# Optimization experiments

Hardware: AMD Instinct MI355X
Metric: run time of the kernel (lower is better)

## Reference

```python
import jax, jax.numpy as jnp
import numpy as np

N = 50000
D_IN = 128
HID = 128
HEADS = 4
PER_HEAD = HID // HEADS
NEG_SLOPE = 0.2


def gatv2_conv(x, src, dst, W_l, W_r, att, bias, H, C, n):
    """PyG GATv2Conv: x [n,F], src/dst [E] (self-loops already appended).
    out[i] = sum_{j->i} softmax_i(att . leaky_relu(Wl x_j + Wr x_i)) * (Wl x_j)
    """
    x_l = (x @ W_l).reshape(n, H, C)  # source-side transform
    x_r = (x @ W_r).reshape(n, H, C)  # destination-side transform
    e = jax.nn.leaky_relu(x_l[src] + x_r[dst], NEG_SLOPE)      # [E,H,C]
    alpha = jnp.einsum('ehc,hc->eh', e, att)                    # [E,H]
    # segment softmax over incoming edges of each destination node
    seg_max = jax.ops.segment_max(alpha, dst, num_segments=n)   # [n,H]
    alpha = jnp.exp(alpha - seg_max[dst])
    denom = jax.ops.segment_sum(alpha, dst, num_segments=n)     # [n,H]
    alpha = alpha / denom[dst]
    msg = x_l[src] * alpha[..., None]                           # [E,H,C]
    out = jax.ops.segment_sum(msg, dst, num_segments=n)         # [n,H,C]
    return out.reshape(n, H * C) + bias


def setup_inputs() -> dict:
    key = jax.random.key(0)
    ks = jax.random.split(key, 10)
    E = 800000
    x = jax.random.normal(ks[0], (N, D_IN), dtype=jnp.float32)
    edge_index = jax.random.randint(ks[1], (2, E), 0, N, dtype=jnp.int64)

    def glorot(k, shape):
        lim = float(np.sqrt(6.0 / (shape[0] + shape[1])))
        return jax.random.uniform(k, shape, jnp.float32, -lim, lim)

    # layer 1: GATv2Conv(D_IN, PER_HEAD, heads=HEADS, concat=True)
    W_l1 = glorot(ks[2], (D_IN, HEADS * PER_HEAD))
    W_r1 = glorot(ks[3], (D_IN, HEADS * PER_HEAD))
    att1 = glorot(ks[4], (HEADS, PER_HEAD))
    b1 = jnp.zeros((HEADS * PER_HEAD,), jnp.float32)
    # layer 2: GATv2Conv(HID, HID, heads=1, concat=True)
    W_l2 = glorot(ks[5], (HID, HID))
    W_r2 = glorot(ks[6], (HID, HID))
    att2 = glorot(ks[7], (1, HID))
    b2 = jnp.zeros((HID,), jnp.float32)
    return {"x": x, "edge_index": edge_index,
            "W_l1": W_l1, "W_r1": W_r1, "att1": att1, "b1": b1,
            "W_l2": W_l2, "W_r2": W_r2, "att2": att2, "b2": b2}


def reference(x, edge_index, W_l1, W_r1, att1, b1, W_l2, W_r2, att2, b2):
    # add self-loops (PyG GATv2Conv default add_self_loops=True)
    loops = jnp.arange(N, dtype=edge_index.dtype)
    src = jnp.concatenate([edge_index[0], loops])
    dst = jnp.concatenate([edge_index[1], loops])
    h = gatv2_conv(x, src, dst, W_l1, W_r1, att1, b1, HEADS, PER_HEAD, N)
    h = jax.nn.relu(h)
    out = gatv2_conv(h, src, dst, W_l2, W_r2, att2, b2, 1, HID, N)
    return out
```

## Files before the change

### kernel.cpp

```cpp
#include <hip/hip_runtime.h>
#include <hip/hip_fp16.h>
#include <math.h>


#define NEG_SLOPE 0.2f
#define CHUNKS 128
#define DCAP 8192

typedef _Float16 half8 __attribute__((ext_vector_type(8)));
typedef _Float16 half2v __attribute__((ext_vector_type(2)));
typedef float floatx4 __attribute__((ext_vector_type(4)));

#if defined(__has_builtin)
#if __has_builtin(__builtin_amdgcn_fdot2)
#define HAVE_FDOT2 1
#endif
#endif

template <int CTRL>
__device__ __forceinline__ float dppmov(float x) {
    int xi = __builtin_bit_cast(int, x);
    int r  = __builtin_amdgcn_update_dpp(0, xi, CTRL, 0xF, 0xF, true);
    return __builtin_bit_cast(float, r);
}
#define DPP_XOR1  0xB1
#define DPP_XOR2  0x4E
#define DPP_HMIRR 0x141
#define DPP_MIRR  0x140


__device__ __forceinline__ void sortA_body(int c, const int* __restrict__ dstA,
                                           int* __restrict__ hist_mat,
                                           int E, int Et, int csz) {
    __shared__ int hist[256];
    int tid = threadIdx.x;
    hist[tid] = 0;
    __syncthreads();
    int start = c * csz, stop = min(Et, start + csz);
    for (int e = start + tid; e < stop; e += 256) {
        int d = (e < E) ? dstA[e] : (e - E);
        atomicAdd(&hist[d >> 8], 1);
    }
    __syncthreads();
    hist_mat[tid * CHUNKS + c] = hist[tid];
}

__device__ __forceinline__ void convert_body(int t,
        const float* __restrict__ Wl1, const float* __restrict__ Wr1,
        const float* __restrict__ Wl2, const float* __restrict__ Wr2,
        const float* __restrict__ att1, const float* __restrict__ att2,
        _Float16* __restrict__ Wt1, _Float16* __restrict__ Wt2,
        _Float16* __restrict__ attH) {
    if (t < 65536) {
        int layer = t >> 15;
        int id = t & 32767;
        int c = id >> 7, k = id & 127;
        const float* Wl = layer ? Wl2 : Wl1;
        const float* Wr = layer ? Wr2 : Wr1;
        _Float16* Wt = layer ? Wt2 : Wt1;
        float v = (c < 128) ? Wl[(size_t)k * 128 + c] : Wr[(size_t)k * 128 + (c - 128)];
        Wt[(size_t)c * 128 + k] = (_Float16)v;
    } else {
        int id = t - 65536;
        if (id < 256) {
            float v = (id < 128) ? att1[id] : att2[id - 128];
            attH[id] = (_Float16)v;
        }
    }
}

__device__ __forceinline__ void scan256_body(const int* __restrict__ hist_mat,
                                             int* __restrict__ offs_flat) {
    __shared__ int wsum[4];
    int t = threadIdx.x;
    int lane = t & 63, w = t >> 6;
    const int4* hp = (const int4*)hist_mat + t * 32;
    int local = 0;
    #pragma unroll 8
    for (int j = 0; j < 32; ++j) {
        int4 v = hp[j];
        local += v.x + v.y + v.z + v.w;
    }
    int x = local;
    #pragma unroll
    for (int off = 1; off < 64; off <<= 1) {
        int y = __shfl_up(x, off, 64);
        if (lane >= off) x += y;
    }
    if (lane == 63) wsum[w] = x;
    __syncthreads();
    int woff = 0;
    for (int i = 0; i < w; ++i) woff += wsum[i];
    int run = woff + x - local;
    int4* op = (int4*)offs_flat + t * 32;
    #pragma unroll 8
    for (int j = 0; j < 32; ++j) {
        int4 v = hp[j];
        int4 o;
        o.x = run;
        o.y = run + v.x;
        o.z = o.y + v.y;
        o.w = o.z + v.z;
        run = o.w + v.w;
        op[j] = o;
    }
}

__device__ __forceinline__ void sortC_body(int c, const int* __restrict__ srcA,
        const int* __restrict__ dstA, const int* __restrict__ offs_flat,
        int* __restrict__ packed, int E, int Et, int csz) {
    __shared__ int pos[256];
    int tid = threadIdx.x;
    pos[tid] = offs_flat[tid * CHUNKS + c];
    __syncthreads();
    int start = c * csz, stop = min(Et, start + csz);
    for (int e = start + tid; e < stop; e += 256) {
        int s, d;
        if (e < E) { s = srcA[e]; d = dstA[e]; } else { s = e - E; d = s; }
        int p = atomicAdd(&pos[d >> 8], 1);
        packed[p] = ((d & 255) << 16) | s;
    }
}

#define BPAD 136

template <bool AF32>
__device__ __forceinline__ void gemm_body(int bid, const void* __restrict__ Av,
        const _Float16* __restrict__ Bt, _Float16* __restrict__ outL,
        _Float16* __restrict__ outR, int n) {
    __shared__ _Float16 sB[256 * BPAD];
    int tid = threadIdx.x;
    {
        int c0 = (tid & 15) * 8;
        int r0 = tid >> 4;
        #pragma unroll
        for (int i = 0; i < 16; ++i) {
            int r = r0 + i * 16;
            *(half8*)(sB + r * BPAD + c0) = *(const half8*)(Bt + (size_t)r * 128 + c0);
        }
    }
    int wave = tid >> 6;
    int lane = tid & 63;
    int ln = lane & 15;
    int q  = lane >> 4;
    int row0 = bid * 64 + wave * 16;

    int arow = row0 + ln;
    if (arow >= n) arow = n - 1;
    half8 a0, a1, a2, a3;
    if (AF32) {
        const float* ap = (const float*)Av + (size_t)arow * 128 + q * 8;
        #pragma unroll
        for (int g = 0; g < 4; ++g) {
            float4 f0 = *(const float4*)(ap + g * 32);
            float4 f1 = *(const float4*)(ap + g * 32 + 4);
            half8 h;
            h[0] = (_Float16)f0.x; h[1] = (_Float16)f0.y;
            h[2] = (_Float16)f0.z; h[3] = (_Float16)f0.w;
            h[4] = (_Float16)f1.x; h[5] = (_Float16)f1.y;
            h[6] = (_Float16)f1.z; h[7] = (_Float16)f1.w;
            if (g == 0) a0 = h; else if (g == 1) a1 = h;
            else if (g == 2) a2 = h; else a3 = h;
        }
    } else {
        const _Float16* ap = (const _Float16*)Av + (size_t)arow * 128 + q * 8;
        a0 = *(const half8*)(ap);
        a1 = *(const half8*)(ap + 32);
        a2 = *(const half8*)(ap + 64);
        a3 = *(const half8*)(ap + 96);
    }

    __syncthreads();

    floatx4 acc[16];
    #pragma unroll
    for (int ct = 0; ct < 16; ++ct) {
        const _Float16* bp = sB + (ct * 16 + ln) * BPAD + q * 8;
        half8 b0 = *(const half8*)(bp);
        half8 b1 = *(const half8*)(bp + 32);
        half8 b2 = *(const half8*)(bp + 64);
        half8 b3 = *(const half8*)(bp + 96);
        floatx4 c = {0.f, 0.f, 0.f, 0.f};
        c = __builtin_amdgcn_mfma_f32_16x16x32_f16(a0, b0, c, 0, 0, 0);
        c = __builtin_amdgcn_mfma_f32_16x16x32_f16(a1, b1, c, 0, 0, 0);
        c = __builtin_amdgcn_mfma_f32_16x16x32_f16(a2, b2, c, 0, 0, 0);
        c = __builtin_amdgcn_mfma_f32_16x16x32_f16(a3, b3, c, 0, 0, 0);
        acc[ct] = c;
    }

    #pragma unroll
    for (int ct = 0; ct < 16; ++ct) {
        int col = ct * 16 + ln;
        #pragma unroll
        for (int r = 0; r < 4; ++r) {
            int grow = row0 + q * 4 + r;
            if (grow < n) {
                _Float16 v = (_Float16)acc[ct][r];
                if (ct < 8) outL[(size_t)grow * 128 + col] = v;
                else        outR[(size_t)grow * 128 + (col - 128)] = v;
            }
        }
    }
}


__global__ __launch_bounds__(256)
void fused_pre(const int* __restrict__ dstA, int* __restrict__ hist_mat,
               int E, int Et, int csz,
               const float* __restrict__ Wl1, const float* __restrict__ Wr1,
               const float* __restrict__ Wl2, const float* __restrict__ Wr2,
               const float* __restrict__ att1, const float* __restrict__ att2,
               _Float16* __restrict__ Wt1, _Float16* __restrict__ Wt2,
               _Float16* __restrict__ attH) {
    if (blockIdx.x < CHUNKS) {
        sortA_body(blockIdx.x, dstA, hist_mat, E, Et, csz);
    } else {
        int t = (blockIdx.x - CHUNKS) * 256 + threadIdx.x;
        convert_body(t, Wl1, Wr1, Wl2, Wr2, att1, att2, Wt1, Wt2, attH);
    }
}

__global__ __launch_bounds__(256)
void fused_scan_gemm(const int* __restrict__ hist_mat, int* __restrict__ offs_flat,
                     const float* __restrict__ X, const _Float16* __restrict__ Wt1,
                     _Float16* __restrict__ outL, _Float16* __restrict__ outR, int n) {
    if (blockIdx.x == 0) {
        scan256_body(hist_mat, offs_flat);
    } else {
        gemm_body<true>(blockIdx.x - 1, X, Wt1, outL, outR, n);
    }
}

__global__ __launch_bounds__(256)
void fused_mid(const int* __restrict__ srcA, const int* __restrict__ dstA,
               const int* __restrict__ offs_flat, int* __restrict__ packed,
               int E, int Et, int csz, int gemm_base,
               const float* __restrict__ X, const _Float16* __restrict__ Wt1,
               _Float16* __restrict__ outL, _Float16* __restrict__ outR, int n) {
    if (blockIdx.x < CHUNKS) {
        sortC_body(blockIdx.x, srcA, dstA, offs_flat, packed, E, Et, csz);
    } else {
        gemm_body<true>(blockIdx.x - CHUNKS + gemm_base, X, Wt1, outL, outR, n);
    }
}

__global__ __launch_bounds__(256)
void gemm_l2(const _Float16* __restrict__ A, const _Float16* __restrict__ Bt,
             _Float16* __restrict__ outL, _Float16* __restrict__ outR, int n) {
    gemm_body<false>(blockIdx.x, A, Bt, outL, outR, n);
}

__global__ __launch_bounds__(256)
void sortD_fine(const int* __restrict__ offs_flat, const int* __restrict__ packed,
                int* __restrict__ rowptr, int* __restrict__ srcs,
                int n, int Et, int nbuck) {
    __shared__ int stage[DCAP];
    __shared__ int sorted[DCAP];
    __shared__ int hist[256], curv[256], wsumD[4];
    int tid = threadIdx.x, b = blockIdx.x;
    int base = offs_flat[b * CHUNKS];
    int end  = (b == nbuck - 1) ? Et : offs_flat[(b + 1) * CHUNKS];
    int m = min(end - base, DCAP);

    hist[tid] = 0;
    for (int i = tid; i < m; i += 256) stage[i] = packed[base + i];
    __syncthreads();
    for (int i = tid; i < m; i += 256) atomicAdd(&hist[stage[i] >> 16], 1);
    __syncthreads();
    {
        int v = hist[tid];
        int lane = tid & 63, w = tid >> 6;
        int x = v;
        #pragma unroll
        for (int off = 1; off < 64; off <<= 1) {
            int y = __shfl_up(x, off, 64);
            if (lane >= off) x += y;
        }
        if (lane == 63) wsumD[w] = x;
        __syncthreads();
        int woff = 0;
        for (int i = 0; i < w; ++i) woff += wsumD[i];
        int excl = woff + x - v;
        curv[tid] = excl;
        int node0 = b << 8;
        if (node0 + tid < n) rowptr[node0 + tid] = base + excl;
        if (b == 0 && tid == 0) rowptr[n] = Et;
    }
    __syncthreads();
    for (int i = tid; i < m; i += 256) {
        int p = stage[i];
        int pos = atomicAdd(&curv[p >> 16], 1);
        sorted[pos] = p & 0xFFFF;
    }
    __syncthreads();
    for (int i = tid; i < m; i += 256) srcs[base + i] = sorted[i];
}


template <bool LAYER1>
__global__ __launch_bounds__(256)
void edge_aggregate(const _Float16* __restrict__ xl, const _Float16* __restrict__ xr,
                    const _Float16* __restrict__ attH, const float* __restrict__ bias,
                    const int* __restrict__ rowptr, const int* __restrict__ srcs,
                    void* __restrict__ outv, int n) {
    int node = blockIdx.x * (blockDim.x >> 6) + (threadIdx.x >> 6);
    int lane = threadIdx.x & 63;
    if (node >= n) return;
    int ln = lane & 15;
    int q  = lane >> 4;
    int c0 = ln * 8;

    half8 xrh = *(const half8*)(xr + (size_t)node * 128 + c0);
    half8 ahh = *(const half8*)(attH + c0);

    float acc[8] = {0.f, 0.f, 0.f, 0.f, 0.f, 0.f, 0.f, 0.f};
    float l = 0.f;

    auto proc = [&](half8 vh, bool valid) {
        half8 e  = vh + xrh;
        half8 es = e * (_Float16)NEG_SLOPE;
        half8 lr = __builtin_elementwise_max(e, es);
        float p = 0.f;
        #pragma unroll
        for (int k = 0; k < 4; ++k) {
            half2v ee = { lr[2 * k], lr[2 * k + 1] };
            half2v aa = { ahh[2 * k], ahh[2 * k + 1] };
#ifdef HAVE_FDOT2
            p = __builtin_amdgcn_fdot2(ee, aa, p, false);
#else
            p = fmaf((float)ee[0], (float)aa[0], p);
            p = fmaf((float)ee[1], (float)aa[1], p);
#endif
        }
        p += dppmov<DPP_XOR1>(p);
        p += dppmov<DPP_XOR2>(p);
        if (!LAYER1) { p += dppmov<DPP_HMIRR>(p); p += dppmov<DPP_MIRR>(p); }
        float pe = __expf(p);
        if (!valid) pe = 0.f;
        l += pe;
        #pragma unroll
        for (int k = 0; k < 8; ++k) acc[k] = fmaf(pe, (float)vh[k], acc[k]);
    };

    int jb = rowptr[node], je = rowptr[node + 1];
    for (int base = jb; base < je; base += 64) {
        int idx = base + lane;
        int myS = (idx < je) ? srcs[idx] : 0;
        int cnt = min(64, je - base);
        int t = 0;
        for (; t + 16 <= cnt; t += 16) {
            int s0 = __shfl(myS, t + q, 64);
            int s1 = __shfl(myS, t + 4 + q, 64);
            int s2 = __shfl(myS, t + 8 + q, 64);
            int s3 = __shfl(myS, t + 12 + q, 64);
            half8 v0 = *(const half8*)(xl + (size_t)s0 * 128 + c0);
            half8 v1 = *(const half8*)(xl + (size_t)s1 * 128 + c0);
            half8 v2 = *(const half8*)(xl + (size_t)s2 * 128 + c0);
            half8 v3 = *(const half8*)(xl + (size_t)s3 * 128 + c0);
            proc(v0, true); proc(v1, true); proc(v2, true); proc(v3, true);
        }
        for (; t < cnt; t += 4) {
            int sa = __shfl(myS, t + q, 64);
            half8 va = *(const half8*)(xl + (size_t)sa * 128 + c0);
            proc(va, (t + q) < cnt);
        }
    }

    #pragma unroll
    for (int k = 0; k < 8; ++k) {
        acc[k] += __shfl_xor(acc[k], 16, 64);
        acc[k] += __shfl_xor(acc[k], 32, 64);
    }
    l += __shfl_xor(l, 16, 64);
    l += __shfl_xor(l, 32, 64);

    float inv = 1.0f / l;
    float bv[8];
    *(float4*)&bv[0] = *(const float4*)(bias + c0);
    *(float4*)&bv[4] = *(const float4*)(bias + c0 + 4);
    float o[8];
    #pragma unroll
    for (int k = 0; k < 8; ++k) {
        o[k] = acc[k] * inv + bv[k];
        if (LAYER1) o[k] = fmaxf(o[k], 0.f);
    }
    if (lane < 16) {
        if (LAYER1) {
            __half2 hh2[4];
            #pragma unroll
            for (int k = 0; k < 4; ++k) hh2[k] = __floats2half2_rn(o[2 * k], o[2 * k + 1]);
            *(float4*)((_Float16*)outv + (size_t)node * 128 + c0) = *(float4*)&hh2[0];
        } else {
            float* out = (float*)outv;
            *(float4*)(out + (size_t)node * 128 + c0)     = *(float4*)&o[0];
            *(float4*)(out + (size_t)node * 128 + c0 + 4) = *(float4*)&o[4];
        }
    }
}


extern "C" void kernel_launch(void* const* d_in, const int* in_sizes, int n_in,
                              void* d_out, int out_size, void* d_ws, size_t ws_size,
                              hipStream_t stream) {
    const float* x    = (const float*)d_in[0];
    const int*   ei   = (const int*)d_in[1];
    const float* Wl1  = (const float*)d_in[2];
    const float* Wr1  = (const float*)d_in[3];
    const float* att1 = (const float*)d_in[4];
    const float* b1   = (const float*)d_in[5];
    const float* Wl2  = (const float*)d_in[6];
    const float* Wr2  = (const float*)d_in[7];
    const float* att2 = (const float*)d_in[8];
    const float* b2   = (const float*)d_in[9];

    int n  = in_sizes[0] / 128;
    int E  = in_sizes[1] / 2;
    int Et = E + n;

    _Float16* xlh  = (_Float16*)d_ws;
    _Float16* xrh2 = xlh + (size_t)n * 128;
    _Float16* hh   = xrh2 + (size_t)n * 128;
    _Float16* Wt1  = hh  + (size_t)n * 128;
    _Float16* Wt2  = Wt1 + 256 * 128;
    _Float16* attH = Wt2 + 256 * 128;
    int* rowptr   = (int*)(attH + 256);
    int* srcs     = rowptr + ((n + 4) & ~3);
    int* packed   = srcs + Et;
    int* hist_mat = packed + Et;
    int* offs_flat= hist_mat + CHUNKS * 256;

    const int* srcA = ei;
    const int* dstA = ei + E;

    int csz   = (Et + CHUNKS - 1) / CHUNKS;
    int nbuck = (n + 255) >> 8;
    int gemm_grid = (n + 63) / 64;
    int edge_grid = (n + 3) / 4;
    int GA = gemm_grid >> 1;
    int GB = gemm_grid - GA;

    fused_pre<<<CHUNKS + 257, 256, 0, stream>>>(
        dstA, hist_mat, E, Et, csz,
        Wl1, Wr1, Wl2, Wr2, att1, att2, Wt1, Wt2, attH);
    fused_scan_gemm<<<1 + GA, 256, 0, stream>>>(
        hist_mat, offs_flat, x, Wt1, xlh, xrh2, n);
    fused_mid<<<CHUNKS + GB, 256, 0, stream>>>(
        srcA, dstA, offs_flat, packed, E, Et, csz, GA,
        x, Wt1, xlh, xrh2, n);
    sortD_fine<<<nbuck, 256, 0, stream>>>(offs_flat, packed, rowptr, srcs, n, Et, nbuck);
    edge_aggregate<true><<<edge_grid, 256, 0, stream>>>(
        xlh, xrh2, attH, b1, rowptr, srcs, hh, n);
    gemm_l2<<<gemm_grid, 256, 0, stream>>>(hh, Wt2, xlh, xrh2, n);
    edge_aggregate<false><<<edge_grid, 256, 0, stream>>>(
        xlh, xrh2, attH + 128, b2, rowptr, srcs, d_out, n);
}
```

Baseline: 217.4 us.

## Replace two-level bucket sort with global-atomic counting sort for CSR build

Swaps the two-pass bucket sort (per-chunk 256-bucket histograms, then a per-bucket fine sort in LDS) for a direct counting sort. Per-node degrees are counted with global atomics, a single block scans them into rowptr and a cursor array, and a scatter pass writes sources through global atomics on the cursor. This drops the sortD_fine kernel and the packed intermediate buffer but adds a memset and many contended global atomics. The order of sources within each row becomes nondeterministic, and the scan now runs on a single block over all nodes.

```diff
diff --git a/kernel.cpp b/kernel.cpp
--- a/kernel.cpp
+++ b/kernel.cpp
@@ -4,8 +4,8 @@
 
 
 #define NEG_SLOPE 0.2f
-#define CHUNKS 128
-#define DCAP 8192
+#define COUNTB 128
+#define SCATB  128
 
 typedef _Float16 half8 __attribute__((ext_vector_type(8)));
 typedef _Float16 half2v __attribute__((ext_vector_type(2)));
@@ -29,20 +29,13 @@
 #define DPP_MIRR  0x140
 
 
-__device__ __forceinline__ void sortA_body(int c, const int* __restrict__ dstA,
-                                           int* __restrict__ hist_mat,
-                                           int E, int Et, int csz) {
-    __shared__ int hist[256];
-    int tid = threadIdx.x;
-    hist[tid] = 0;
-    __syncthreads();
-    int start = c * csz, stop = min(Et, start + csz);
-    for (int e = start + tid; e < stop; e += 256) {
+__device__ __forceinline__ void count_body(int b, const int* __restrict__ dstA,
+                                           int* __restrict__ counts, int E, int Et) {
+    const int STR = COUNTB * 256;
+    for (int e = b * 256 + threadIdx.x; e < Et; e += STR) {
         int d = (e < E) ? dstA[e] : (e - E);
-        atomicAdd(&hist[d >> 8], 1);
-    }
-    __syncthreads();
-    hist_mat[tid * CHUNKS + c] = hist[tid];
+        atomicAdd(&counts[d], 1);
+    }
 }
 
 __device__ __forceinline__ void convert_body(int t,
@@ -69,16 +62,16 @@
     }
 }
 
-__device__ __forceinline__ void scan256_body(const int* __restrict__ hist_mat,
-                                             int* __restrict__ offs_flat) {
+__device__ __forceinline__ void scan_body(const int* __restrict__ counts,
+        int* __restrict__ rowptr, int* __restrict__ cursor, int n, int Et) {
     __shared__ int wsum[4];
     int t = threadIdx.x;
     int lane = t & 63, w = t >> 6;
-    const int4* hp = (const int4*)hist_mat + t * 32;
+    int c4 = (n + 1023) >> 10;
+    const int4* cp = (const int4*)counts + (size_t)t * c4;
     int local = 0;
-    #pragma unroll 8
-    for (int j = 0; j < 32; ++j) {
-        int4 v = hp[j];
+    for (int j = 0; j < c4; ++j) {
+        int4 v = cp[j];
         local += v.x + v.y + v.z + v.w;
     }
     int x = local;
@@ -92,33 +85,48 @@
     int woff = 0;
     for (int i = 0; i < w; ++i) woff += wsum[i];
     int run = woff + x - local;
-    int4* op = (int4*)offs_flat + t * 32;
-    #pragma unroll 8
-    for (int j = 0; j < 32; ++j) {
-        int4 v = hp[j];
+    int4* rp = (int4*)rowptr + (size_t)t * c4;
+    int4* qp = (int4*)cursor + (size_t)t * c4;
+    for (int j = 0; j < c4; ++j) {
+        int4 v = cp[j];
         int4 o;
         o.x = run;
         o.y = run + v.x;
         o.z = o.y + v.y;
         o.w = o.z + v.z;
         run = o.w + v.w;
-        op[j] = o;
-    }
-}
-
-__device__ __forceinline__ void sortC_body(int c, const int* __restrict__ srcA,
-        const int* __restrict__ dstA, const int* __restrict__ offs_flat,
-        int* __restrict__ packed, int E, int Et, int csz) {
-    __shared__ int pos[256];
-    int tid = threadIdx.x;
-    pos[tid] = offs_flat[tid * CHUNKS + c];
-    __syncthreads();
-    int start = c * csz, stop = min(Et, start + csz);
-    for (int e = start + tid; e < stop; e += 256) {
+        rp[j] = o;
+        qp[j] = o;
+    }
+    if (t == 255) rowptr[n] = Et;
+}
+
+__device__ __forceinline__ void scatter_body(int b, const int* __restrict__ srcA,
+        const int* __restrict__ dstA, int* __restrict__ cursor,
+        int* __restrict__ srcs, int E, int Et) {
+    const int STR = SCATB * 256;
+    int e = b * 256 + threadIdx.x;
+    for (; e + 3 * STR < Et; e += 4 * STR) {
+        int ea = e, eb = e + STR, ec = e + 2 * STR, ed = e + 3 * STR;
+        int s0, d0, s1, d1, s2, d2, s3, d3;
+        if (ea < E) { s0 = srcA[ea]; d0 = dstA[ea]; } else { s0 = ea - E; d0 = s0; }
+        if (eb < E) { s1 = srcA[eb]; d1 = dstA[eb]; } else { s1 = eb - E; d1 = s1; }
+        if (ec < E) { s2 = srcA[ec]; d2 = dstA[ec]; } else { s2 = ec - E; d2 = s2; }
+        if (ed < E) { s3 = srcA[ed]; d3 = dstA[ed]; } else { s3 = ed - E; d3 = s3; }
+        int p0 = atomicAdd(&cursor[d0], 1);
+        int p1 = atomicAdd(&cursor[d1], 1);
+        int p2 = atomicAdd(&cursor[d2], 1);
+        int p3 = atomicAdd(&cursor[d3], 1);
+        srcs[p0] = s0;
+        srcs[p1] = s1;
+        srcs[p2] = s2;
+        srcs[p3] = s3;
+    }
+    for (; e < Et; e += STR) {
         int s, d;
         if (e < E) { s = srcA[e]; d = dstA[e]; } else { s = e - E; d = s; }
-        int p = atomicAdd(&pos[d >> 8], 1);
-        packed[p] = ((d & 255) << 16) | s;
+        int p = atomicAdd(&cursor[d], 1);
+        srcs[p] = s;
     }
 }
 
@@ -205,42 +213,45 @@
 
 
 __global__ __launch_bounds__(256)
-void fused_pre(const int* __restrict__ dstA, int* __restrict__ hist_mat,
-               int E, int Et, int csz,
+void fused_pre(const int* __restrict__ dstA, int* __restrict__ counts,
+               int E, int Et,
                const float* __restrict__ Wl1, const float* __restrict__ Wr1,
                const float* __restrict__ Wl2, const float* __restrict__ Wr2,
                const float* __restrict__ att1, const float* __restrict__ att2,
                _Float16* __restrict__ Wt1, _Float16* __restrict__ Wt2,
                _Float16* __restrict__ attH) {
-    if (blockIdx.x < CHUNKS) {
-        sortA_body(blockIdx.x, dstA, hist_mat, E, Et, csz);
+    if (blockIdx.x < COUNTB) {
+        count_body(blockIdx.x, dstA, counts, E, Et);
     } else {
-        int t = (blockIdx.x - CHUNKS) * 256 + threadIdx.x;
+        int t = (blockIdx.x - COUNTB) * 256 + threadIdx.x;
         convert_body(t, Wl1, Wr1, Wl2, Wr2, att1, att2, Wt1, Wt2, attH);
     }
 }
 
 __global__ __launch_bounds__(256)
-void fused_scan_gemm(const int* __restrict__ hist_mat, int* __restrict__ offs_flat,
+void fused_scan_gemm(const int* __restrict__ counts, int* __restrict__ rowptr,
+                     int* __restrict__ cursor,
                      const float* __restrict__ X, const _Float16* __restrict__ Wt1,
-                     _Float16* __restrict__ outL, _Float16* __restrict__ outR, int n) {
+                     _Float16* __restrict__ outL, _Float16* __restrict__ outR,
+                     int n, int Et) {
     if (blockIdx.x == 0) {
-        scan256_body(hist_mat, offs_flat);
+        scan_body(counts, rowptr, cursor, n, Et);
     } else {
         gemm_body<true>(blockIdx.x - 1, X, Wt1, outL, outR, n);
     }
 }
 
 __global__ __launch_bounds__(256)
-void fused_mid(const int* __restrict__ srcA, const int* __restrict__ dstA,
-               const int* __restrict__ offs_flat, int* __restrict__ packed,
-               int E, int Et, int csz, int gemm_base,
-               const float* __restrict__ X, const _Float16* __restrict__ Wt1,
-               _Float16* __restrict__ outL, _Float16* __restrict__ outR, int n) {
-    if (blockIdx.x < CHUNKS) {
-        sortC_body(blockIdx.x, srcA, dstA, offs_flat, packed, E, Et, csz);
+void fused_scatter_gemm(const int* __restrict__ srcA, const int* __restrict__ dstA,
+                        int* __restrict__ cursor, int* __restrict__ srcs,
+                        int E, int Et, int gemm_base,
+                        const float* __restrict__ X, const _Float16* __restrict__ Wt1,
+                        _Float16* __restrict__ outL, _Float16* __restrict__ outR,
+                        int n) {
+    if (blockIdx.x < SCATB) {
+        scatter_body(blockIdx.x, srcA, dstA, cursor, srcs, E, Et);
     } else {
-        gemm_body<true>(blockIdx.x - CHUNKS + gemm_base, X, Wt1, outL, outR, n);
+        gemm_body<true>(blockIdx.x - SCATB + gemm_base, X, Wt1, outL, outR, n);
     }
 }
 
@@ -248,52 +259,6 @@
 void gemm_l2(const _Float16* __restrict__ A, const _Float16* __restrict__ Bt,
              _Float16* __restrict__ outL, _Float16* __restrict__ outR, int n) {
     gemm_body<false>(blockIdx.x, A, Bt, outL, outR, n);
-}
-
-__global__ __launch_bounds__(256)
-void sortD_fine(const int* __restrict__ offs_flat, const int* __restrict__ packed,
-                int* __restrict__ rowptr, int* __restrict__ srcs,
-                int n, int Et, int nbuck) {
-    __shared__ int stage[DCAP];
-    __shared__ int sorted[DCAP];
-    __shared__ int hist[256], curv[256], wsumD[4];
-    int tid = threadIdx.x, b = blockIdx.x;
-    int base = offs_flat[b * CHUNKS];
-    int end  = (b == nbuck - 1) ? Et : offs_flat[(b + 1) * CHUNKS];
-    int m = min(end - base, DCAP);
-
-    hist[tid] = 0;
-    for (int i = tid; i < m; i += 256) stage[i] = packed[base + i];
-    __syncthreads();
-    for (int i = tid; i < m; i += 256) atomicAdd(&hist[stage[i] >> 16], 1);
-    __syncthreads();
-    {
-        int v = hist[tid];
-        int lane = tid & 63, w = tid >> 6;
-        int x = v;
-        #pragma unroll
-        for (int off = 1; off < 64; off <<= 1) {
-            int y = __shfl_up(x, off, 64);
-            if (lane >= off) x += y;
-        }
-        if (lane == 63) wsumD[w] = x;
-        __syncthreads();
-        int woff = 0;
-        for (int i = 0; i < w; ++i) woff += wsumD[i];
-        int excl = woff + x - v;
-        curv[tid] = excl;
-        int node0 = b << 8;
-        if (node0 + tid < n) rowptr[node0 + tid] = base + excl;
-        if (b == 0 && tid == 0) rowptr[n] = Et;
-    }
-    __syncthreads();
-    for (int i = tid; i < m; i += 256) {
-        int p = stage[i];
-        int pos = atomicAdd(&curv[p >> 16], 1);
-        sorted[pos] = p & 0xFFFF;
-    }
-    __syncthreads();
-    for (int i = tid; i < m; i += 256) srcs[base + i] = sorted[i];
 }
 
 
@@ -416,6 +381,7 @@
     int n  = in_sizes[0] / 128;
     int E  = in_sizes[1] / 2;
     int Et = E + n;
+    int npad = ((n + 1023) >> 10) << 10;
 
     _Float16* xlh  = (_Float16*)d_ws;
     _Float16* xrh2 = xlh + (size_t)n * 128;
@@ -423,31 +389,28 @@
     _Float16* Wt1  = hh  + (size_t)n * 128;
     _Float16* Wt2  = Wt1 + 256 * 128;
     _Float16* attH = Wt2 + 256 * 128;
-    int* rowptr   = (int*)(attH + 256);
-    int* srcs     = rowptr + ((n + 4) & ~3);
-    int* packed   = srcs + Et;
-    int* hist_mat = packed + Et;
-    int* offs_flat= hist_mat + CHUNKS * 256;
+    int* rowptr = (int*)(attH + 256);
+    int* cursor = rowptr + npad + 16;
+    int* counts = cursor + npad;
+    int* srcs   = counts + npad;
 
     const int* srcA = ei;
     const int* dstA = ei + E;
 
-    int csz   = (Et + CHUNKS - 1) / CHUNKS;
-    int nbuck = (n + 255) >> 8;
     int gemm_grid = (n + 63) / 64;
     int edge_grid = (n + 3) / 4;
     int GA = gemm_grid >> 1;
     int GB = gemm_grid - GA;
 
-    fused_pre<<<CHUNKS + 257, 256, 0, stream>>>(
-        dstA, hist_mat, E, Et, csz,
+    hipMemsetAsync(counts, 0, (size_t)npad * sizeof(int), stream);
+    fused_pre<<<COUNTB + 257, 256, 0, stream>>>(
+        dstA, counts, E, Et,
         Wl1, Wr1, Wl2, Wr2, att1, att2, Wt1, Wt2, attH);
     fused_scan_gemm<<<1 + GA, 256, 0, stream>>>(
-        hist_mat, offs_flat, x, Wt1, xlh, xrh2, n);
-    fused_mid<<<CHUNKS + GB, 256, 0, stream>>>(
-        srcA, dstA, offs_flat, packed, E, Et, csz, GA,
+        counts, rowptr, cursor, x, Wt1, xlh, xrh2, n, Et);
+    fused_scatter_gemm<<<SCATB + GB, 256, 0, stream>>>(
+        srcA, dstA, cursor, srcs, E, Et, GA,
         x, Wt1, xlh, xrh2, n);
-    sortD_fine<<<nbuck, 256, 0, stream>>>(offs_flat, packed, rowptr, srcs, n, Et, nbuck);
     edge_aggregate<true><<<edge_grid, 256, 0, stream>>>(
         xlh, xrh2, attH, b1, rowptr, srcs, hh, n);
     gemm_l2<<<gemm_grid, 256, 0, stream>>>(hh, Wt2, xlh, xrh2, n);
```

After: 287.2 us. 32.1% more time.

## Fuse fine bucket sort with layer-1 edge aggregation using 32-node buckets

Applied to the files above, without the earlier changes.

The coarse counting sort now uses 32-node buckets instead of 256-node ones, and 64 chunks instead of 128. The fine sort kernel is merged with the layer-1 attention aggregation, so each block sorts its bucket's sources into shared memory as 16-bit values and aggregates those nodes straight from shared memory. This removes one kernel launch and the global round trip of the sorted source list for layer 1. In exchange, the single-block scan now covers a much larger histogram, and each block's aggregation is limited to 32 nodes, with a shared-memory cap of 1024 edges per bucket.

```diff
diff --git a/kernel.cpp b/kernel.cpp
--- a/kernel.cpp
+++ b/kernel.cpp
@@ -4,8 +4,10 @@
 
 
 #define NEG_SLOPE 0.2f
-#define CHUNKS 128
-#define DCAP 8192
+#define CHUNKS 64
+#define NB 32
+#define NBUCK_PAD 2048
+#define DCAP 1024
 
 typedef _Float16 half8 __attribute__((ext_vector_type(8)));
 typedef _Float16 half2v __attribute__((ext_vector_type(2)));
@@ -32,17 +34,18 @@
 __device__ __forceinline__ void sortA_body(int c, const int* __restrict__ dstA,
                                            int* __restrict__ hist_mat,
                                            int E, int Et, int csz) {
-    __shared__ int hist[256];
+    __shared__ int hist[NBUCK_PAD];
     int tid = threadIdx.x;
-    hist[tid] = 0;
+    for (int k = tid; k < NBUCK_PAD; k += 256) hist[k] = 0;
     __syncthreads();
     int start = c * csz, stop = min(Et, start + csz);
     for (int e = start + tid; e < stop; e += 256) {
         int d = (e < E) ? dstA[e] : (e - E);
-        atomicAdd(&hist[d >> 8], 1);
-    }
-    __syncthreads();
-    hist_mat[tid * CHUNKS + c] = hist[tid];
+        atomicAdd(&hist[d >> 5], 1);
+    }
+    __syncthreads();
+    for (int k = tid; k < NBUCK_PAD; k += 256)
+        hist_mat[k * CHUNKS + c] = hist[k];
 }
 
 __device__ __forceinline__ void convert_body(int t,
@@ -69,15 +72,15 @@
     }
 }
 
-__device__ __forceinline__ void scan256_body(const int* __restrict__ hist_mat,
-                                             int* __restrict__ offs_flat) {
+__device__ __forceinline__ void scan_body(const int* __restrict__ hist_mat,
+                                          int* __restrict__ offs_flat) {
     __shared__ int wsum[4];
     int t = threadIdx.x;
     int lane = t & 63, w = t >> 6;
-    const int4* hp = (const int4*)hist_mat + t * 32;
+    const int4* hp = (const int4*)hist_mat + (size_t)t * 128;
     int local = 0;
     #pragma unroll 8
-    for (int j = 0; j < 32; ++j) {
+    for (int j = 0; j < 128; ++j) {
         int4 v = hp[j];
         local += v.x + v.y + v.z + v.w;
     }
@@ -92,9 +95,9 @@
     int woff = 0;
     for (int i = 0; i < w; ++i) woff += wsum[i];
     int run = woff + x - local;
-    int4* op = (int4*)offs_flat + t * 32;
+    int4* op = (int4*)offs_flat + (size_t)t * 128;
     #pragma unroll 8
-    for (int j = 0; j < 32; ++j) {
+    for (int j = 0; j < 128; ++j) {
         int4 v = hp[j];
         int4 o;
         o.x = run;
@@ -109,16 +112,17 @@
 __device__ __forceinline__ void sortC_body(int c, const int* __restrict__ srcA,
         const int* __restrict__ dstA, const int* __restrict__ offs_flat,
         int* __restrict__ packed, int E, int Et, int csz) {
-    __shared__ int pos[256];
+    __shared__ int pos[NBUCK_PAD];
     int tid = threadIdx.x;
-    pos[tid] = offs_flat[tid * CHUNKS + c];
+    for (int k = tid; k < NBUCK_PAD; k += 256)
+        pos[k] = offs_flat[k * CHUNKS + c];
     __syncthreads();
     int start = c * csz, stop = min(Et, start + csz);
     for (int e = start + tid; e < stop; e += 256) {
         int s, d;
         if (e < E) { s = srcA[e]; d = dstA[e]; } else { s = e - E; d = s; }
-        int p = atomicAdd(&pos[d >> 8], 1);
-        packed[p] = ((d & 255) << 16) | s;
+        int p = atomicAdd(&pos[d >> 5], 1);
+        packed[p] = ((d & 31) << 16) | s;
     }
 }
 
@@ -225,7 +229,7 @@
                      const float* __restrict__ X, const _Float16* __restrict__ Wt1,
                      _Float16* __restrict__ outL, _Float16* __restrict__ outR, int n) {
     if (blockIdx.x == 0) {
-        scan256_body(hist_mat, offs_flat);
+        scan_body(hist_mat, offs_flat);
     } else {
         gemm_body<true>(blockIdx.x - 1, X, Wt1, outL, outR, n);
     }
@@ -250,50 +254,138 @@
     gemm_body<false>(blockIdx.x, A, Bt, outL, outR, n);
 }
 
+
 __global__ __launch_bounds__(256)
-void sortD_fine(const int* __restrict__ offs_flat, const int* __restrict__ packed,
-                int* __restrict__ rowptr, int* __restrict__ srcs,
-                int n, int Et, int nbuck) {
+void sort_agg(const int* __restrict__ offs_flat, const int* __restrict__ packed,
+              int* __restrict__ rowptr, int* __restrict__ srcs,
+              const _Float16* __restrict__ xl, const _Float16* __restrict__ xr,
+              const _Float16* __restrict__ attH, const float* __restrict__ bias,
+              _Float16* __restrict__ out, int n, int Et) {
     __shared__ int stage[DCAP];
-    __shared__ int sorted[DCAP];
-    __shared__ int hist[256], curv[256], wsumD[4];
+    __shared__ unsigned short s16[DCAP];
+    __shared__ int hist[NB];
+    __shared__ int curv[NB];
+    __shared__ int rp_l[NB + 1];
+
     int tid = threadIdx.x, b = blockIdx.x;
     int base = offs_flat[b * CHUNKS];
-    int end  = (b == nbuck - 1) ? Et : offs_flat[(b + 1) * CHUNKS];
+    int end  = offs_flat[(b + 1) * CHUNKS];
     int m = min(end - base, DCAP);
-
-    hist[tid] = 0;
+    int node0 = b * NB;
+
+    if (tid < NB) hist[tid] = 0;
     for (int i = tid; i < m; i += 256) stage[i] = packed[base + i];
     __syncthreads();
     for (int i = tid; i < m; i += 256) atomicAdd(&hist[stage[i] >> 16], 1);
     __syncthreads();
-    {
-        int v = hist[tid];
-        int lane = tid & 63, w = tid >> 6;
+    if (tid < 64) {
+        int lane = tid;
+        int v = (lane < NB) ? hist[lane] : 0;
         int x = v;
         #pragma unroll
         for (int off = 1; off < 64; off <<= 1) {
             int y = __shfl_up(x, off, 64);
             if (lane >= off) x += y;
         }
-        if (lane == 63) wsumD[w] = x;
-        __syncthreads();
-        int woff = 0;
-        for (int i = 0; i < w; ++i) woff += wsumD[i];
-        int excl = woff + x - v;
-        curv[tid] = excl;
-        int node0 = b << 8;
-        if (node0 + tid < n) rowptr[node0 + tid] = base + excl;
-        if (b == 0 && tid == 0) rowptr[n] = Et;
+        if (lane < NB) { rp_l[lane] = x - v; curv[lane] = x - v; }
+        if (lane == NB - 1) rp_l[NB] = x;
     }
     __syncthreads();
     for (int i = tid; i < m; i += 256) {
         int p = stage[i];
         int pos = atomicAdd(&curv[p >> 16], 1);
-        sorted[pos] = p & 0xFFFF;
-    }
-    __syncthreads();
-    for (int i = tid; i < m; i += 256) srcs[base + i] = sorted[i];
+        s16[pos] = (unsigned short)(p & 0xFFFF);
+    }
+    __syncthreads();
+
+    if (tid < NB && node0 + tid < n) rowptr[node0 + tid] = base + rp_l[tid];
+    if (b == 0 && tid == 0) rowptr[n] = Et;
+    for (int i = tid; i < m; i += 256) srcs[base + i] = (int)s16[i];
+
+    int w = tid >> 6, lane = tid & 63;
+    int ln = lane & 15, q = lane >> 4, c0 = ln * 8;
+    half8 ahh = *(const half8*)(attH + c0);
+    float bv[8];
+    *(float4*)&bv[0] = *(const float4*)(bias + c0);
+    *(float4*)&bv[4] = *(const float4*)(bias + c0 + 4);
+
+    for (int i = 0; i < NB / 4; ++i) {
+        int j = w * (NB / 4) + i;
+        int node = node0 + j;
+        if (node >= n) break;
+        half8 xrh = *(const half8*)(xr + (size_t)node * 128 + c0);
+        float acc[8] = {0.f, 0.f, 0.f, 0.f, 0.f, 0.f, 0.f, 0.f};
+        float l = 0.f;
+
+        auto proc = [&](half8 vh, bool valid) {
+            half8 e  = vh + xrh;
+            half8 es = e * (_Float16)NEG_SLOPE;
+            half8 lr = __builtin_elementwise_max(e, es);
+            float p = 0.f;
+            #pragma unroll
+            for (int k = 0; k < 4; ++k) {
+                half2v ee = { lr[2 * k], lr[2 * k + 1] };
+                half2v aa = { ahh[2 * k], ahh[2 * k + 1] };
+#ifdef HAVE_FDOT2
+                p = __builtin_amdgcn_fdot2(ee, aa, p, false);
+#else
+                p = fmaf((float)ee[0], (float)aa[0], p);
+                p = fmaf((float)ee[1], (float)aa[1], p);
+#endif
+            }
+            p += dppmov<DPP_XOR1>(p);
+            p += dppmov<DPP_XOR2>(p);
+            float pe = __expf(p);
+            if (!valid) pe = 0.f;
+            l += pe;
+            #pragma unroll
+            for (int k = 0; k < 8; ++k) acc[k] = fmaf(pe, (float)vh[k], acc[k]);
+        };
+
+        int jb = rp_l[j], je = rp_l[j + 1];
+        for (int be = jb; be < je; be += 64) {
+            int idx = be + lane;
+            int myS = (idx < je) ? (int)s16[idx] : 0;
+            int cnt = min(64, je - be);
+            int t = 0;
+            for (; t + 16 <= cnt; t += 16) {
+                int s0 = __shfl(myS, t + q, 64);
+                int s1 = __shfl(myS, t + 4 + q, 64);
+                int s2 = __shfl(myS, t + 8 + q, 64);
+                int s3 = __shfl(myS, t + 12 + q, 64);
+                half8 v0 = *(const half8*)(xl + (size_t)s0 * 128 + c0);
+                half8 v1 = *(const half8*)(xl + (size_t)s1 * 128 + c0);
+                half8 v2 = *(const half8*)(xl + (size_t)s2 * 128 + c0);
+                half8 v3 = *(const half8*)(xl + (size_t)s3 * 128 + c0);
+                proc(v0, true); proc(v1, true); proc(v2, true); proc(v3, true);
+            }
+            for (; t < cnt; t += 4) {
+                int sa = __shfl(myS, t + q, 64);
+                half8 va = *(const half8*)(xl + (size_t)sa * 128 + c0);
+                proc(va, (t + q) < cnt);
+            }
+        }
+
+        #pragma unroll
+        for (int k = 0; k < 8; ++k) {
+            acc[k] += __shfl_xor(acc[k], 16, 64);
+            acc[k] += __shfl_xor(acc[k], 32, 64);
+        }
+        l += __shfl_xor(l, 16, 64);
+        l += __shfl_xor(l, 32, 64);
+
+        float inv = 1.0f / l;
+        float o[8];
+        #pragma unroll
+        for (int k = 0; k < 8; ++k)
+            o[k] = fmaxf(acc[k] * inv + bv[k], 0.f);
+        if (lane < 16) {
+            __half2 hh2[4];
+            #pragma unroll
+            for (int k = 0; k < 4; ++k) hh2[k] = __floats2half2_rn(o[2 * k], o[2 * k + 1]);
+            *(float4*)(out + (size_t)node * 128 + c0) = *(float4*)&hh2[0];
+        }
+    }
 }
 
 
@@ -424,16 +516,16 @@
     _Float16* Wt2  = Wt1 + 256 * 128;
     _Float16* attH = Wt2 + 256 * 128;
     int* rowptr   = (int*)(attH + 256);
-    int* srcs     = rowptr + ((n + 4) & ~3);
-    int* packed   = srcs + Et;
-    int* hist_mat = packed + Et;
-    int* offs_flat= hist_mat + CHUNKS * 256;
+    int* packed   = rowptr + ((n + 16) & ~3);
+    int* srcs     = packed + Et;
+    int* hist_mat = srcs + Et;
+    int* offs_flat= hist_mat + NBUCK_PAD * CHUNKS;
 
     const int* srcA = ei;
     const int* dstA = ei + E;
 
     int csz   = (Et + CHUNKS - 1) / CHUNKS;
-    int nbuck = (n + 255) >> 8;
+    int nbuck = (n + NB - 1) / NB;
     int gemm_grid = (n + 63) / 64;
     int edge_grid = (n + 3) / 4;
     int GA = gemm_grid >> 1;
@@ -447,9 +539,8 @@
     fused_mid<<<CHUNKS + GB, 256, 0, stream>>>(
         srcA, dstA, offs_flat, packed, E, Et, csz, GA,
         x, Wt1, xlh, xrh2, n);
-    sortD_fine<<<nbuck, 256, 0, stream>>>(offs_flat, packed, rowptr, srcs, n, Et, nbuck);
-    edge_aggregate<true><<<edge_grid, 256, 0, stream>>>(
-        xlh, xrh2, attH, b1, rowptr, srcs, hh, n);
+    sort_agg<<<nbuck, 256, 0, stream>>>(
+        offs_flat, packed, rowptr, srcs, xlh, xrh2, attH, b1, hh, n, Et);
     gemm_l2<<<gemm_grid, 256, 0, stream>>>(hh, Wt2, xlh, xrh2, n);
     edge_aggregate<false><<<edge_grid, 256, 0, stream>>>(
         xlh, xrh2, attH + 128, b2, rowptr, srcs, d_out, n);
```

Result: slower. 282.0 us (+29.7%).

## Fuse fine sort with a third slice of the layer-1 GEMM

Applied to the files above, without the earlier changes.

Splits the layer-1 GEMM into three slices instead of two and runs the last slice inside the fine-bucket sort kernel, so the sort's low-occupancy blocks overlap with GEMM blocks. The sort stage now keeps sorted sources as 16-bit values in dynamic shared memory that it shares with the GEMM's B tile, which fits both in about 68KB. The GEMM now receives its LDS buffer as a parameter. The risk is that the larger dynamic LDS allocation on every block limits occupancy, and that the GEMM slices may be unevenly balanced against the sort work.

```diff
diff --git a/kernel.cpp b/kernel.cpp
--- a/kernel.cpp
+++ b/kernel.cpp
@@ -122,13 +122,60 @@
     }
 }
 
+__device__ __forceinline__ void sortD_body(int b, const int* __restrict__ offs_flat,
+        const int* __restrict__ packed, int* __restrict__ rowptr,
+        int* __restrict__ srcs, int n, int Et, int nbuck, char* smem) {
+    int* stage = (int*)smem;
+    unsigned short* s16 = (unsigned short*)(smem + DCAP * 4);
+    int* hist  = (int*)(smem + DCAP * 6);
+    int* curv  = hist + 256;
+    int* wsumD = curv + 256;
+    int tid = threadIdx.x;
+    int base = offs_flat[b * CHUNKS];
+    int end  = (b == nbuck - 1) ? Et : offs_flat[(b + 1) * CHUNKS];
+    int m = min(end - base, DCAP);
+
+    hist[tid] = 0;
+    for (int i = tid; i < m; i += 256) stage[i] = packed[base + i];
+    __syncthreads();
+    for (int i = tid; i < m; i += 256) atomicAdd(&hist[stage[i] >> 16], 1);
+    __syncthreads();
+    {
+        int v = hist[tid];
+        int lane = tid & 63, w = tid >> 6;
+        int x = v;
+        #pragma unroll
+        for (int off = 1; off < 64; off <<= 1) {
+            int y = __shfl_up(x, off, 64);
+            if (lane >= off) x += y;
+        }
+        if (lane == 63) wsumD[w] = x;
+        __syncthreads();
+        int woff = 0;
+        for (int i = 0; i < w; ++i) woff += wsumD[i];
+        int excl = woff + x - v;
+        curv[tid] = excl;
+        int node0 = b << 8;
+        if (node0 + tid < n) rowptr[node0 + tid] = base + excl;
+        if (b == 0 && tid == 0) rowptr[n] = Et;
+    }
+    __syncthreads();
+    for (int i = tid; i < m; i += 256) {
+        int p = stage[i];
+        int pos = atomicAdd(&curv[p >> 16], 1);
+        s16[pos] = (unsigned short)(p & 0xFFFF);
+    }
+    __syncthreads();
+    for (int i = tid; i < m; i += 256) srcs[base + i] = (int)s16[i];
+}
+
 #define BPAD 136
+#define GEMM_LDS_BYTES (256 * BPAD * 2)
 
 template <bool AF32>
 __device__ __forceinline__ void gemm_body(int bid, const void* __restrict__ Av,
         const _Float16* __restrict__ Bt, _Float16* __restrict__ outL,
-        _Float16* __restrict__ outR, int n) {
-    __shared__ _Float16 sB[256 * BPAD];
+        _Float16* __restrict__ outR, int n, _Float16* sB) {
     int tid = threadIdx.x;
     {
         int c0 = (tid & 15) * 8;
@@ -224,10 +271,11 @@
 void fused_scan_gemm(const int* __restrict__ hist_mat, int* __restrict__ offs_flat,
                      const float* __restrict__ X, const _Float16* __restrict__ Wt1,
                      _Float16* __restrict__ outL, _Float16* __restrict__ outR, int n) {
+    __shared__ _Float16 sB[256 * BPAD];
     if (blockIdx.x == 0) {
         scan256_body(hist_mat, offs_flat);
     } else {
-        gemm_body<true>(blockIdx.x - 1, X, Wt1, outL, outR, n);
+        gemm_body<true>(blockIdx.x - 1, X, Wt1, outL, outR, n, sB);
     }
 }
 
@@ -237,63 +285,34 @@
                int E, int Et, int csz, int gemm_base,
                const float* __restrict__ X, const _Float16* __restrict__ Wt1,
                _Float16* __restrict__ outL, _Float16* __restrict__ outR, int n) {
+    __shared__ _Float16 sB[256 * BPAD];
     if (blockIdx.x < CHUNKS) {
         sortC_body(blockIdx.x, srcA, dstA, offs_flat, packed, E, Et, csz);
     } else {
-        gemm_body<true>(blockIdx.x - CHUNKS + gemm_base, X, Wt1, outL, outR, n);
+        gemm_body<true>(blockIdx.x - CHUNKS + gemm_base, X, Wt1, outL, outR, n, sB);
+    }
+}
+
+__global__ __launch_bounds__(256)
+void fused_sortD_gemm(const int* __restrict__ offs_flat, const int* __restrict__ packed,
+                      int* __restrict__ rowptr, int* __restrict__ srcs,
+                      int n, int Et, int nbuck, int gemm_base,
+                      const float* __restrict__ X, const _Float16* __restrict__ Wt1,
+                      _Float16* __restrict__ outL, _Float16* __restrict__ outR) {
+    extern __shared__ char smem[];
+    if (blockIdx.x < nbuck) {
+        sortD_body(blockIdx.x, offs_flat, packed, rowptr, srcs, n, Et, nbuck, smem);
+    } else {
+        gemm_body<true>(blockIdx.x - nbuck + gemm_base, X, Wt1, outL, outR, n,
+                        (_Float16*)smem);
     }
 }
 
 __global__ __launch_bounds__(256)
 void gemm_l2(const _Float16* __restrict__ A, const _Float16* __restrict__ Bt,
              _Float16* __restrict__ outL, _Float16* __restrict__ outR, int n) {
-    gemm_body<false>(blockIdx.x, A, Bt, outL, outR, n);
-}
-
-__global__ __launch_bounds__(256)
-void sortD_fine(const int* __restrict__ offs_flat, const int* __restrict__ packed,
-                int* __restrict__ rowptr, int* __restrict__ srcs,
-                int n, int Et, int nbuck) {
-    __shared__ int stage[DCAP];
-    __shared__ int sorted[DCAP];
-    __shared__ int hist[256], curv[256], wsumD[4];
-    int tid = threadIdx.x, b = blockIdx.x;
-    int base = offs_flat[b * CHUNKS];
-    int end  = (b == nbuck - 1) ? Et : offs_flat[(b + 1) * CHUNKS];
-    int m = min(end - base, DCAP);
-
-    hist[tid] = 0;
-    for (int i = tid; i < m; i += 256) stage[i] = packed[base + i];
-    __syncthreads();
-    for (int i = tid; i < m; i += 256) atomicAdd(&hist[stage[i] >> 16], 1);
-    __syncthreads();
-    {
-        int v = hist[tid];
-        int lane = tid & 63, w = tid >> 6;
-        int x = v;
-        #pragma unroll
-        for (int off = 1; off < 64; off <<= 1) {
-            int y = __shfl_up(x, off, 64);
-            if (lane >= off) x += y;
-        }
-        if (lane == 63) wsumD[w] = x;
-        __syncthreads();
-        int woff = 0;
-        for (int i = 0; i < w; ++i) woff += wsumD[i];
-        int excl = woff + x - v;
-        curv[tid] = excl;
-        int node0 = b << 8;
-        if (node0 + tid < n) rowptr[node0 + tid] = base + excl;
-        if (b == 0 && tid == 0) rowptr[n] = Et;
-    }
-    __syncthreads();
-    for (int i = tid; i < m; i += 256) {
-        int p = stage[i];
-        int pos = atomicAdd(&curv[p >> 16], 1);
-        sorted[pos] = p & 0xFFFF;
-    }
-    __syncthreads();
-    for (int i = tid; i < m; i += 256) srcs[base + i] = sorted[i];
+    __shared__ _Float16 sB[256 * BPAD];
+    gemm_body<false>(blockIdx.x, A, Bt, outL, outR, n, sB);
 }
 
 
@@ -436,8 +455,9 @@
     int nbuck = (n + 255) >> 8;
     int gemm_grid = (n + 63) / 64;
     int edge_grid = (n + 3) / 4;
-    int GA = gemm_grid >> 1;
-    int GB = gemm_grid - GA;
+    int GA = gemm_grid / 3;
+    int GB = gemm_grid / 3;
+    int GC = gemm_grid - GA - GB;
 
     fused_pre<<<CHUNKS + 257, 256, 0, stream>>>(
         dstA, hist_mat, E, Et, csz,
@@ -447,7 +467,9 @@
     fused_mid<<<CHUNKS + GB, 256, 0, stream>>>(
         srcA, dstA, offs_flat, packed, E, Et, csz, GA,
         x, Wt1, xlh, xrh2, n);
-    sortD_fine<<<nbuck, 256, 0, stream>>>(offs_flat, packed, rowptr, srcs, n, Et, nbuck);
+    fused_sortD_gemm<<<nbuck + GC, 256, GEMM_LDS_BYTES, stream>>>(
+        offs_flat, packed, rowptr, srcs, n, Et, nbuck, GA + GB,
+        x, Wt1, xlh, xrh2);
     edge_aggregate<true><<<edge_grid, 256, 0, stream>>>(
         xlh, xrh2, attH, b1, rowptr, srcs, hh, n);
     gemm_l2<<<gemm_grid, 256, 0, stream>>>(hh, Wt2, xlh, xrh2, n);
```

Result: slower. 224.2 us (+3.1%).
